# Optimization experiments

Measured on AMD Instinct MI355X. Metric: run time of the kernel, lower is better.

The kernel has to match this reference:

```python
import jax, jax.numpy as jnp
import numpy as np

N = 100000  # nodes
E = 1600000  # edges
F_IN = 512
H = 128
C = 40
L = 8
ALPHA = 0.1
THETA = 0.5


def setup_inputs() -> dict:
    key = jax.random.key(0)
    ks = jax.random.split(key, 8)
    x = jax.random.normal(ks[0], (N, F_IN), dtype=jnp.float32)
    edge_index = jax.random.randint(ks[1], (2, E), 0, N, dtype=jnp.int32)
    edge_weight = jax.random.uniform(ks[2], (E,), dtype=jnp.float32)
    W0 = jax.random.normal(ks[3], (F_IN, H), dtype=jnp.float32) * 0.05
    b0 = jnp.zeros((H,), dtype=jnp.float32)
    convW = jax.random.normal(ks[4], (L, H, H), dtype=jnp.float32) * 0.05
    W1 = jax.random.normal(ks[5], (H, C), dtype=jnp.float32) * 0.05
    b1 = jnp.zeros((C,), dtype=jnp.float32)
    return {"x": x, "edge_index": edge_index, "edge_weight": edge_weight,
            "W0": W0, "b0": b0, "convW": convW, "W1": W1, "b1": b1}


def reference(x, edge_index, edge_weight, W0, b0, convW, W1, b1):
    # eval mode, dropout=0.0 -> dropout is identity
    src, dst = edge_index[0], edge_index[1]
    h = jnp.maximum(x @ W0 + b0, 0.0)  # [N, H]
    x0 = h  # initial residual
    # GCN2Conv beta per layer: log(theta/layer + 1), layer = 1..L
    betas = jnp.log(THETA / jnp.arange(1, L + 1, dtype=jnp.float32) + 1.0)

    def layer(h, inputs):
        W, beta = inputs  # W: [H, H]
        # sparse adjacency propagation: sum_j A_ij * h_j
        msgs = h[src] * edge_weight[:, None]  # [E, H]
        agg = jax.ops.segment_sum(msgs, dst, num_segments=N)  # [N, H]
        # initial residual mixing + identity mapping (shared_weights=True)
        out = (1.0 - ALPHA) * agg + ALPHA * x0
        out = (1.0 - beta) * out + beta * (out @ W)
        return jnp.maximum(out, 0.0), None

    h, _ = jax.lax.scan(layer, h, (convW, betas))
    logits = h @ W1 + b1  # [N, C]
    return jax.nn.log_softmax(logits, axis=-1)
```

## Files before the change

### kernel.cpp

```cpp
#include <hip/hip_runtime.h>
#include <hip/hip_bf16.h>
#include <cmath>

#define NN 100000
#define NE 1600000
#define FIN 512
#define HD 128
#define NC 40
#define NL 8

typedef __attribute__((ext_vector_type(8))) short bh8;
typedef __attribute__((ext_vector_type(4))) float f4;
typedef __attribute__((ext_vector_type(4))) unsigned int u4;

__device__ __forceinline__ float bflo(unsigned p){ return __uint_as_float(p << 16); }
__device__ __forceinline__ float bfhi(unsigned p){ return __uint_as_float(p & 0xffff0000u); }
__device__ __forceinline__ unsigned short f2bf(float f){
  unsigned u = __float_as_uint(f);
  u += 0x7fffu + ((u >> 16) & 1u);
  return (unsigned short)(u >> 16);
}
__device__ __forceinline__ unsigned pack2(float a, float b){
  return (unsigned)f2bf(a) | ((unsigned)f2bf(b) << 16);
}

__global__ void k_deg(const int* __restrict__ dst, int* __restrict__ deg, int e){
  for (int i = blockIdx.x * blockDim.x + threadIdx.x; i < e; i += gridDim.x * blockDim.x)
    atomicAdd(&deg[dst[i]], 1);
}

__global__ void k_scan(const int* __restrict__ deg, int* __restrict__ offs,
                       int* __restrict__ cur, int n){
  __shared__ int wsum[16];
  __shared__ int carry;
  int t = threadIdx.x, lane = t & 63, wid = t >> 6;
  if (t == 0) carry = 0;
  __syncthreads();
  for (int base = 0; base < n; base += 1024){
    int idx = base + t;
    int v = (idx < n) ? deg[idx] : 0;
    int orig = v;
    #pragma unroll
    for (int off = 1; off < 64; off <<= 1){
      int u = __shfl_up(v, off);
      if (lane >= off) v += u;
    }
    if (lane == 63) wsum[wid] = v;
    __syncthreads();
    if (wid == 0){
      int s = (lane < 16) ? wsum[lane] : 0;
      #pragma unroll
      for (int off = 1; off < 16; off <<= 1){
        int u = __shfl_up(s, off);
        if (lane >= off) s += u;
      }
      if (lane < 16) wsum[lane] = s;
    }
    __syncthreads();
    int wexcl = (wid == 0) ? 0 : wsum[wid - 1];
    int excl = carry + wexcl + (v - orig);
    if (idx < n){ offs[idx] = excl; cur[idx] = excl; }
    int ctot = wsum[15];
    __syncthreads();
    if (t == 0) carry += ctot;
    __syncthreads();
  }
  if (t == 0) offs[n] = carry;
}

__global__ void k_scatter(const int* __restrict__ src, const int* __restrict__ dst,
                          const float* __restrict__ w, int* __restrict__ cur,
                          int* __restrict__ csrc, float* __restrict__ cw, int e){
  for (int i = blockIdx.x * blockDim.x + threadIdx.x; i < e; i += gridDim.x * blockDim.x){
    int d = dst[i];
    int p = atomicAdd(&cur[d], 1);
    csrc[p] = src[i];
    cw[p] = w[i];
  }
}

__global__ void k_twt(const float* __restrict__ in, unsigned short* __restrict__ out,
                      int K, int C, int Cpad){
  int total = Cpad * K;
  for (int i = blockIdx.x * blockDim.x + threadIdx.x; i < total; i += gridDim.x * blockDim.x){
    int c = i / K, k = i % K;
    float v = (c < C) ? in[(size_t)k * C + c] : 0.f;
    out[i] = f2bf(v);
  }
}

__global__ __launch_bounds__(256) void k_gemm0(const float* __restrict__ X,
                                               const unsigned short* __restrict__ Wt,
                                               const float* __restrict__ b0,
                                               unsigned* __restrict__ Ha,
                                               unsigned* __restrict__ Hb, int n){
  __shared__ __attribute__((aligned(16))) char lds[33792];
  char* ldsA = lds;
  char* ldsW = lds + 8192;
  float* ldsO = (float*)lds;
  int t = threadIdx.x;
  int w = t >> 6, lane = t & 63;
  int rowBase = blockIdx.x * 64;
  f4 acc[8];
  #pragma unroll
  for (int i = 0; i < 8; i++) acc[i] = (f4)0.f;

  for (int kk = 0; kk < 8; kk++){
    #pragma unroll
    for (int iter = 0; iter < 2; iter++){
      int r = t / 8 + iter * 32;
      int kc = (t % 8) * 8;
      int grow = rowBase + r;
      float4 f0 = {0,0,0,0}, f1 = {0,0,0,0};
      if (grow < n){
        const float4* p = (const float4*)(X + (size_t)grow * FIN + kk * 64 + kc);
        f0 = p[0]; f1 = p[1];
      }
      u4 pv = { pack2(f0.x, f0.y), pack2(f0.z, f0.w), pack2(f1.x, f1.y), pack2(f1.z, f1.w) };
      *(u4*)(ldsA + r * 128 + ((kc * 2) ^ ((r & 7) << 4))) = pv;
    }
    #pragma unroll
    for (int iter = 0; iter < 4; iter++){
      int c = t / 8 + iter * 32;
      int kc = (t % 8) * 8;
      bh8 v = *(const bh8*)(Wt + (size_t)c * FIN + kk * 64 + kc);
      *(bh8*)(ldsW + c * 128 + ((kc * 2) ^ ((c & 7) << 4))) = v;
    }
    __syncthreads();
    int rowf = (w << 4) + (lane & 15);
    #pragma unroll
    for (int ks = 0; ks < 2; ks++){
      bh8 fa = *(const bh8*)(ldsA + rowf * 128 + ((ks * 64 + (lane >> 4) * 16) ^ ((rowf & 7) << 4)));
      #pragma unroll
      for (int ct = 0; ct < 8; ct++){
        int colf = (ct << 4) + (lane & 15);
        bh8 fb = *(const bh8*)(ldsW + colf * 128 + ((ks * 64 + (lane >> 4) * 16) ^ ((colf & 7) << 4)));
        acc[ct] = __builtin_amdgcn_mfma_f32_16x16x32_bf16(fa, fb, acc[ct], 0, 0, 0);
      }
    }
    __syncthreads();
  }
  #pragma unroll
  for (int ct = 0; ct < 8; ct++){
    int colf = (ct << 4) + (lane & 15);
    float bb = b0[colf];
    #pragma unroll
    for (int i = 0; i < 4; i++){
      int r = (w << 4) + ((lane >> 4) << 2) + i;
      float v = acc[ct][i] + bb;
      ldsO[r * 132 + colf] = v > 0.f ? v : 0.f;
    }
  }
  __syncthreads();
  #pragma unroll
  for (int iter = 0; iter < 4; iter++){
    int r = iter * 16 + t / 16;
    int c8 = (t % 16) * 8;
    int grow = rowBase + r;
    if (grow < n){
      float* p = &ldsO[r * 132 + c8];
      u4 pv = { pack2(p[0], p[1]), pack2(p[2], p[3]), pack2(p[4], p[5]), pack2(p[6], p[7]) };
      *(u4*)(Ha + (size_t)grow * 64 + (t % 16) * 4) = pv;
      *(u4*)(Hb + (size_t)grow * 64 + (t % 16) * 4) = pv;
    }
  }
}

__global__ __launch_bounds__(256) void k_agg(const unsigned* __restrict__ H,
                                             const unsigned* __restrict__ X0,
                                             const int* __restrict__ offs,
                                             const int* __restrict__ csrc,
                                             const float* __restrict__ cw,
                                             unsigned* __restrict__ T, int n){
  int gw = (blockIdx.x * blockDim.x + threadIdx.x) >> 6;
  int lane = threadIdx.x & 63;
  int q = lane >> 4, l16 = lane & 15;
  int nw = (gridDim.x * blockDim.x) >> 6;
  for (int d = gw; d < n; d += nw){
    int e0 = offs[d], e1 = offs[d + 1];
    float a0=0.f,a1=0.f,a2=0.f,a3=0.f,a4=0.f,a5=0.f,a6=0.f,a7=0.f;
    for (int e = e0 + q; e < e1; e += 4){
      int s = csrc[e]; float wq = cw[e];
      u4 p = *(const u4*)(H + (size_t)s * 64 + l16 * 4);
      a0 += wq * bflo(p.x); a1 += wq * bfhi(p.x);
      a2 += wq * bflo(p.y); a3 += wq * bfhi(p.y);
      a4 += wq * bflo(p.z); a5 += wq * bfhi(p.z);
      a6 += wq * bflo(p.w); a7 += wq * bfhi(p.w);
    }
    a0 += __shfl_xor(a0,16); a0 += __shfl_xor(a0,32);
    a1 += __shfl_xor(a1,16); a1 += __shfl_xor(a1,32);
    a2 += __shfl_xor(a2,16); a2 += __shfl_xor(a2,32);
    a3 += __shfl_xor(a3,16); a3 += __shfl_xor(a3,32);
    a4 += __shfl_xor(a4,16); a4 += __shfl_xor(a4,32);
    a5 += __shfl_xor(a5,16); a5 += __shfl_xor(a5,32);
    a6 += __shfl_xor(a6,16); a6 += __shfl_xor(a6,32);
    a7 += __shfl_xor(a7,16); a7 += __shfl_xor(a7,32);
    if (q == 0){
      u4 xp = *(const u4*)(X0 + (size_t)d * 64 + l16 * 4);
      float v0 = 0.9f*a0 + 0.1f*bflo(xp.x), v1 = 0.9f*a1 + 0.1f*bfhi(xp.x);
      float v2 = 0.9f*a2 + 0.1f*bflo(xp.y), v3 = 0.9f*a3 + 0.1f*bfhi(xp.y);
      float v4 = 0.9f*a4 + 0.1f*bflo(xp.z), v5 = 0.9f*a5 + 0.1f*bfhi(xp.z);
      float v6 = 0.9f*a6 + 0.1f*bflo(xp.w), v7 = 0.9f*a7 + 0.1f*bfhi(xp.w);
      u4 ov = { pack2(v0,v1), pack2(v2,v3), pack2(v4,v5), pack2(v6,v7) };
      *(u4*)(T + (size_t)d * 64 + l16 * 4) = ov;
    }
  }
}

__global__ __launch_bounds__(256) void k_gemmL(const unsigned short* __restrict__ A,
                                               const unsigned short* __restrict__ Wt,
                                               float beta,
                                               unsigned* __restrict__ Hout, int n){
  __shared__ __attribute__((aligned(16))) char lds[49152];
  char* ldsA = lds;
  char* ldsW = lds + 16384;
  float* ldsO = (float*)lds;
  int t = threadIdx.x;
  int w = t >> 6, lane = t & 63;
  int rowBase = blockIdx.x * 64;

  #pragma unroll
  for (int iter = 0; iter < 4; iter++){
    int r = t / 16 + iter * 16;
    int kc = (t % 16) * 8;
    int grow = rowBase + r;
    bh8 v = (bh8)(short)0;
    if (grow < n) v = *(const bh8*)(A + (size_t)grow * HD + kc);
    *(bh8*)(ldsA + r * 256 + ((kc * 2) ^ ((r & 7) << 4))) = v;
  }
  #pragma unroll
  for (int iter = 0; iter < 8; iter++){
    int c = t / 16 + iter * 16;
    int kc = (t % 16) * 8;
    bh8 v = *(const bh8*)(Wt + (size_t)c * HD + kc);
    *(bh8*)(ldsW + c * 256 + ((kc * 2) ^ ((c & 7) << 4))) = v;
  }
  __syncthreads();

  f4 acc[8];
  #pragma unroll
  for (int i = 0; i < 8; i++) acc[i] = (f4)0.f;
  int rowf = (w << 4) + (lane & 15);
  #pragma unroll
  for (int ks = 0; ks < 4; ks++){
    bh8 fa = *(const bh8*)(ldsA + rowf * 256 + ((ks * 64 + (lane >> 4) * 16) ^ ((rowf & 7) << 4)));
    #pragma unroll
    for (int ct = 0; ct < 8; ct++){
      int colf = (ct << 4) + (lane & 15);
      bh8 fb = *(const bh8*)(ldsW + colf * 256 + ((ks * 64 + (lane >> 4) * 16) ^ ((colf & 7) << 4)));
      acc[ct] = __builtin_amdgcn_mfma_f32_16x16x32_bf16(fa, fb, acc[ct], 0, 0, 0);
    }
  }

  float vout[8][4];
  #pragma unroll
  for (int ct = 0; ct < 8; ct++){
    int colf = (ct << 4) + (lane & 15);
    #pragma unroll
    for (int i = 0; i < 4; i++){
      int r = (w << 4) + ((lane >> 4) << 2) + i;
      unsigned short tv = *(const unsigned short*)(ldsA + r * 256 + ((colf * 2) ^ ((r & 7) << 4)));
      float tf = __uint_as_float(((unsigned)tv) << 16);
      float v = (1.f - beta) * tf + beta * acc[ct][i];
      vout[ct][i] = v > 0.f ? v : 0.f;
    }
  }
  __syncthreads();
  #pragma unroll
  for (int ct = 0; ct < 8; ct++){
    int colf = (ct << 4) + (lane & 15);
    #pragma unroll
    for (int i = 0; i < 4; i++){
      int r = (w << 4) + ((lane >> 4) << 2) + i;
      ldsO[r * 132 + colf] = vout[ct][i];
    }
  }
  __syncthreads();
  #pragma unroll
  for (int iter = 0; iter < 4; iter++){
    int r = iter * 16 + t / 16;
    int c8 = (t % 16) * 8;
    int grow = rowBase + r;
    if (grow < n){
      float* p = &ldsO[r * 132 + c8];
      u4 pv = { pack2(p[0], p[1]), pack2(p[2], p[3]), pack2(p[4], p[5]), pack2(p[6], p[7]) };
      *(u4*)(Hout + (size_t)grow * 64 + (t % 16) * 4) = pv;
    }
  }
}

__global__ __launch_bounds__(256) void k_final(const unsigned* __restrict__ H,
                                               const unsigned short* __restrict__ W1t,
                                               const float* __restrict__ b1,
                                               float* __restrict__ out, int n){
  __shared__ __attribute__((aligned(16))) char lds[16384 + 12288];
  char* ldsA = lds;
  char* ldsW = lds + 16384;
  int t = threadIdx.x;
  int w = t >> 6, lane = t & 63;
  int l15 = lane & 15;
  int rowBase = blockIdx.x * 64;
  const unsigned short* Hs = (const unsigned short*)H;

  #pragma unroll
  for (int iter = 0; iter < 4; iter++){
    int r = t / 16 + iter * 16;
    int kc = (t % 16) * 8;
    int grow = rowBase + r;
    bh8 v = (bh8)(short)0;
    if (grow < n) v = *(const bh8*)(Hs + (size_t)grow * HD + kc);
    *(bh8*)(ldsA + r * 256 + ((kc * 2) ^ ((r & 7) << 4))) = v;
  }
  #pragma unroll
  for (int iter = 0; iter < 3; iter++){
    int c = t / 16 + iter * 16;
    int kc = (t % 16) * 8;
    bh8 v = *(const bh8*)(W1t + (size_t)c * HD + kc);
    *(bh8*)(ldsW + c * 256 + ((kc * 2) ^ ((c & 7) << 4))) = v;
  }
  __syncthreads();

  f4 acc[3];
  #pragma unroll
  for (int i = 0; i < 3; i++) acc[i] = (f4)0.f;
  int rowf = (w << 4) + l15;
  #pragma unroll
  for (int ks = 0; ks < 4; ks++){
    bh8 fa = *(const bh8*)(ldsA + rowf * 256 + ((ks * 64 + (lane >> 4) * 16) ^ ((rowf & 7) << 4)));
    #pragma unroll
    for (int ct = 0; ct < 3; ct++){
      int colf = (ct << 4) + l15;
      bh8 fb = *(const bh8*)(ldsW + colf * 256 + ((ks * 64 + (lane >> 4) * 16) ^ ((colf & 7) << 4)));
      acc[ct] = __builtin_amdgcn_mfma_f32_16x16x32_bf16(fa, fb, acc[ct], 0, 0, 0);
    }
  }

  float bias0 = b1[l15];
  float bias1 = b1[16 + l15];
  bool v2ok = (l15 < 8);
  float bias2 = v2ok ? b1[32 + l15] : 0.f;

  #pragma unroll
  for (int i = 0; i < 4; i++){
    int r = rowBase + (w << 4) + ((lane >> 4) << 2) + i;
    float v0 = acc[0][i] + bias0;
    float v1 = acc[1][i] + bias1;
    float v2 = v2ok ? (acc[2][i] + bias2) : -1e30f;
    float m = fmaxf(fmaxf(v0, v1), v2);
    #pragma unroll
    for (int off = 1; off < 16; off <<= 1) m = fmaxf(m, __shfl_xor(m, off));
    float e0 = __expf(v0 - m), e1 = __expf(v1 - m);
    float e2 = v2ok ? __expf(v2 - m) : 0.f;
    float s = e0 + e1 + e2;
    #pragma unroll
    for (int off = 1; off < 16; off <<= 1) s += __shfl_xor(s, off);
    float ls = m + __logf(s);
    if (r < n){
      out[(size_t)r * NC + l15] = v0 - ls;
      out[(size_t)r * NC + 16 + l15] = v1 - ls;
      if (v2ok) out[(size_t)r * NC + 32 + l15] = v2 - ls;
    }
  }
}

extern "C" void kernel_launch(void* const* d_in, const int* in_sizes, int n_in,
                              void* d_out, int out_size, void* d_ws, size_t ws_size,
                              hipStream_t stream){
  const float* x  = (const float*)d_in[0];
  const int*   ei = (const int*)d_in[1];
  const float* ew = (const float*)d_in[2];
  const float* W0 = (const float*)d_in[3];
  const float* b0 = (const float*)d_in[4];
  const float* cW = (const float*)d_in[5];
  const float* W1 = (const float*)d_in[6];
  const float* b1 = (const float*)d_in[7];
  float* out = (float*)d_out;
  const int* src = ei;
  const int* dst = ei + NE;

  char* ws = (char*)d_ws;
  size_t off = 0;
  auto alloc = [&](size_t bytes) -> char* {
    char* p = ws + off;
    off += (bytes + 255) & ~(size_t)255;
    return p;
  };
  unsigned* x0b = (unsigned*)alloc((size_t)NN * 64 * 4);
  unsigned* hb  = (unsigned*)alloc((size_t)NN * 64 * 4);
  unsigned* tb  = (unsigned*)alloc((size_t)NN * 64 * 4);
  unsigned short* W0t = (unsigned short*)alloc((size_t)FIN * HD * 2);
  unsigned short* cWt = (unsigned short*)alloc((size_t)NL * HD * HD * 2);
  unsigned short* W1t = (unsigned short*)alloc((size_t)48 * HD * 2);
  int*   deg  = (int*)alloc((size_t)NN * 4);
  int*   offs = (int*)alloc((size_t)(NN + 1) * 4);
  int*   cur  = (int*)alloc((size_t)NN * 4);
  int*   csrc = (int*)alloc((size_t)NE * 4);
  float* cwv  = (float*)alloc((size_t)NE * 4);

  (void)hipMemsetAsync(deg, 0, (size_t)NN * 4, stream);
  hipLaunchKernelGGL(k_deg, dim3(1024), dim3(256), 0, stream, dst, deg, NE);
  hipLaunchKernelGGL(k_scan, dim3(1), dim3(1024), 0, stream, deg, offs, cur, NN);
  hipLaunchKernelGGL(k_scatter, dim3(1024), dim3(256), 0, stream, src, dst, ew, cur, csrc, cwv, NE);
  hipLaunchKernelGGL(k_twt, dim3(256), dim3(256), 0, stream, W0, W0t, FIN, HD, HD);
  for (int l = 0; l < NL; l++)
    hipLaunchKernelGGL(k_twt, dim3(64), dim3(256), 0, stream,
                       cW + (size_t)l * HD * HD, cWt + (size_t)l * HD * HD, HD, HD, HD);
  hipLaunchKernelGGL(k_twt, dim3(24), dim3(256), 0, stream, W1, W1t, HD, NC, 48);

  int gblocks = (NN + 63) / 64;
  hipLaunchKernelGGL(k_gemm0, dim3(gblocks), dim3(256), 0, stream, x, W0t, b0, x0b, hb, NN);
  for (int l = 0; l < NL; l++){
    float beta = logf(0.5f / (float)(l + 1) + 1.0f);
    hipLaunchKernelGGL(k_agg, dim3(2048), dim3(256), 0, stream, hb, x0b, offs, csrc, cwv, tb, NN);
    hipLaunchKernelGGL(k_gemmL, dim3(gblocks), dim3(256), 0, stream,
                       (const unsigned short*)tb, cWt + (size_t)l * HD * HD, beta, hb, NN);
  }
  hipLaunchKernelGGL(k_final, dim3(gblocks), dim3(256), 0, stream, hb, W1t, b1, out, NN);
}
```

Baseline: 1.049 ms.

## Fuse sparse aggregation into per-layer GEMM kernel and pack edge src/weight

Merges the per-layer aggregation and dense GEMM into one kernel. Each block aggregates its 64 rows straight into LDS, then runs the MFMA GEMM with ping-pong H buffers, so the intermediate T tensor is never written to or read back from global memory. Edge source index and weight are packed into one 8-byte record, and the gather loop is unrolled by two to keep more loads in flight. The trade-off is a fixed 64-rows-per-block schedule instead of a grid-stride warp loop, which can cause load imbalance across blocks and lower occupancy from the larger LDS footprint.

```diff
diff --git a/kernel.cpp b/kernel.cpp
--- a/kernel.cpp
+++ b/kernel.cpp
@@ -12,6 +12,7 @@
 typedef __attribute__((ext_vector_type(8))) short bh8;
 typedef __attribute__((ext_vector_type(4))) float f4;
 typedef __attribute__((ext_vector_type(4))) unsigned int u4;
+typedef __attribute__((ext_vector_type(2))) unsigned int u2;
 
 __device__ __forceinline__ float bflo(unsigned p){ return __uint_as_float(p << 16); }
 __device__ __forceinline__ float bfhi(unsigned p){ return __uint_as_float(p & 0xffff0000u); }
@@ -70,12 +71,12 @@
 
 __global__ void k_scatter(const int* __restrict__ src, const int* __restrict__ dst,
                           const float* __restrict__ w, int* __restrict__ cur,
-                          int* __restrict__ csrc, float* __restrict__ cw, int e){
+                          u2* __restrict__ epk, int e){
   for (int i = blockIdx.x * blockDim.x + threadIdx.x; i < e; i += gridDim.x * blockDim.x){
     int d = dst[i];
     int p = atomicAdd(&cur[d], 1);
-    csrc[p] = src[i];
-    cw[p] = w[i];
+    u2 v = { (unsigned)src[i], __float_as_uint(w[i]) };
+    epk[p] = v;
   }
 }
 
@@ -166,26 +167,59 @@
   }
 }
 
-__global__ __launch_bounds__(256) void k_agg(const unsigned* __restrict__ H,
-                                             const unsigned* __restrict__ X0,
-                                             const int* __restrict__ offs,
-                                             const int* __restrict__ csrc,
-                                             const float* __restrict__ cw,
-                                             unsigned* __restrict__ T, int n){
-  int gw = (blockIdx.x * blockDim.x + threadIdx.x) >> 6;
-  int lane = threadIdx.x & 63;
+__global__ __launch_bounds__(256) void k_layer(const unsigned* __restrict__ Hin,
+                                               const unsigned* __restrict__ X0,
+                                               const int* __restrict__ offs,
+                                               const u2* __restrict__ epk,
+                                               const unsigned short* __restrict__ Wt,
+                                               float beta,
+                                               unsigned* __restrict__ Hout, int n){
+  __shared__ __attribute__((aligned(16))) char lds[49152];
+  char* ldsA = lds;
+  char* ldsW = lds + 16384;
+  float* ldsO = (float*)lds;
+  int t = threadIdx.x;
+  int w = t >> 6, lane = t & 63;
   int q = lane >> 4, l16 = lane & 15;
-  int nw = (gridDim.x * blockDim.x) >> 6;
-  for (int d = gw; d < n; d += nw){
+  int rowBase = blockIdx.x * 64;
+
+  #pragma unroll
+  for (int iter = 0; iter < 8; iter++){
+    int c = t / 16 + iter * 16;
+    int kc = (t % 16) * 8;
+    bh8 v = *(const bh8*)(Wt + (size_t)c * HD + kc);
+    *(bh8*)(ldsW + c * 256 + ((kc * 2) ^ ((c & 7) << 4))) = v;
+  }
+
+  for (int i = 0; i < 16; i++){
+    int lr = (w << 4) + i;
+    int d = rowBase + lr;
+    if (d >= n) continue;
     int e0 = offs[d], e1 = offs[d + 1];
     float a0=0.f,a1=0.f,a2=0.f,a3=0.f,a4=0.f,a5=0.f,a6=0.f,a7=0.f;
-    for (int e = e0 + q; e < e1; e += 4){
-      int s = csrc[e]; float wq = cw[e];
-      u4 p = *(const u4*)(H + (size_t)s * 64 + l16 * 4);
-      a0 += wq * bflo(p.x); a1 += wq * bfhi(p.x);
-      a2 += wq * bflo(p.y); a3 += wq * bfhi(p.y);
-      a4 += wq * bflo(p.z); a5 += wq * bfhi(p.z);
-      a6 += wq * bflo(p.w); a7 += wq * bfhi(p.w);
+    int e = e0 + q;
+    for (; e + 4 < e1; e += 8){
+      u2 p0 = epk[e], p1 = epk[e + 4];
+      float w0 = __uint_as_float(p0.y), w1 = __uint_as_float(p1.y);
+      u4 r0 = *(const u4*)(Hin + (size_t)p0.x * 64 + l16 * 4);
+      u4 r1 = *(const u4*)(Hin + (size_t)p1.x * 64 + l16 * 4);
+      a0 += w0 * bflo(r0.x) + w1 * bflo(r1.x);
+      a1 += w0 * bfhi(r0.x) + w1 * bfhi(r1.x);
+      a2 += w0 * bflo(r0.y) + w1 * bflo(r1.y);
+      a3 += w0 * bfhi(r0.y) + w1 * bfhi(r1.y);
+      a4 += w0 * bflo(r0.z) + w1 * bflo(r1.z);
+      a5 += w0 * bfhi(r0.z) + w1 * bfhi(r1.z);
+      a6 += w0 * bflo(r0.w) + w1 * bflo(r1.w);
+      a7 += w0 * bfhi(r0.w) + w1 * bfhi(r1.w);
+    }
+    if (e < e1){
+      u2 p0 = epk[e];
+      float w0 = __uint_as_float(p0.y);
+      u4 r0 = *(const u4*)(Hin + (size_t)p0.x * 64 + l16 * 4);
+      a0 += w0 * bflo(r0.x); a1 += w0 * bfhi(r0.x);
+      a2 += w0 * bflo(r0.y); a3 += w0 * bfhi(r0.y);
+      a4 += w0 * bflo(r0.z); a5 += w0 * bfhi(r0.z);
+      a6 += w0 * bflo(r0.w); a7 += w0 * bfhi(r0.w);
     }
     a0 += __shfl_xor(a0,16); a0 += __shfl_xor(a0,32);
     a1 += __shfl_xor(a1,16); a1 += __shfl_xor(a1,32);
@@ -202,38 +236,8 @@
       float v4 = 0.9f*a4 + 0.1f*bflo(xp.z), v5 = 0.9f*a5 + 0.1f*bfhi(xp.z);
       float v6 = 0.9f*a6 + 0.1f*bflo(xp.w), v7 = 0.9f*a7 + 0.1f*bfhi(xp.w);
       u4 ov = { pack2(v0,v1), pack2(v2,v3), pack2(v4,v5), pack2(v6,v7) };
-      *(u4*)(T + (size_t)d * 64 + l16 * 4) = ov;
-    }
-  }
-}
-
-__global__ __launch_bounds__(256) void k_gemmL(const unsigned short* __restrict__ A,
-                                               const unsigned short* __restrict__ Wt,
-                                               float beta,
-                                               unsigned* __restrict__ Hout, int n){
-  __shared__ __attribute__((aligned(16))) char lds[49152];
-  char* ldsA = lds;
-  char* ldsW = lds + 16384;
-  float* ldsO = (float*)lds;
-  int t = threadIdx.x;
-  int w = t >> 6, lane = t & 63;
-  int rowBase = blockIdx.x * 64;
-
-  #pragma unroll
-  for (int iter = 0; iter < 4; iter++){
-    int r = t / 16 + iter * 16;
-    int kc = (t % 16) * 8;
-    int grow = rowBase + r;
-    bh8 v = (bh8)(short)0;
-    if (grow < n) v = *(const bh8*)(A + (size_t)grow * HD + kc);
-    *(bh8*)(ldsA + r * 256 + ((kc * 2) ^ ((r & 7) << 4))) = v;
-  }
-  #pragma unroll
-  for (int iter = 0; iter < 8; iter++){
-    int c = t / 16 + iter * 16;
-    int kc = (t % 16) * 8;
-    bh8 v = *(const bh8*)(Wt + (size_t)c * HD + kc);
-    *(bh8*)(ldsW + c * 256 + ((kc * 2) ^ ((c & 7) << 4))) = v;
+      *(u4*)(ldsA + lr * 256 + ((l16 * 16) ^ ((lr & 7) << 4))) = ov;
+    }
   }
   __syncthreads();
 
@@ -386,21 +390,20 @@
     return p;
   };
   unsigned* x0b = (unsigned*)alloc((size_t)NN * 64 * 4);
-  unsigned* hb  = (unsigned*)alloc((size_t)NN * 64 * 4);
-  unsigned* tb  = (unsigned*)alloc((size_t)NN * 64 * 4);
+  unsigned* hbA = (unsigned*)alloc((size_t)NN * 64 * 4);
+  unsigned* hbB = (unsigned*)alloc((size_t)NN * 64 * 4);
   unsigned short* W0t = (unsigned short*)alloc((size_t)FIN * HD * 2);
   unsigned short* cWt = (unsigned short*)alloc((size_t)NL * HD * HD * 2);
   unsigned short* W1t = (unsigned short*)alloc((size_t)48 * HD * 2);
   int*   deg  = (int*)alloc((size_t)NN * 4);
   int*   offs = (int*)alloc((size_t)(NN + 1) * 4);
   int*   cur  = (int*)alloc((size_t)NN * 4);
-  int*   csrc = (int*)alloc((size_t)NE * 4);
-  float* cwv  = (float*)alloc((size_t)NE * 4);
+  u2*    epk  = (u2*)alloc((size_t)NE * 8);
 
   (void)hipMemsetAsync(deg, 0, (size_t)NN * 4, stream);
   hipLaunchKernelGGL(k_deg, dim3(1024), dim3(256), 0, stream, dst, deg, NE);
   hipLaunchKernelGGL(k_scan, dim3(1), dim3(1024), 0, stream, deg, offs, cur, NN);
-  hipLaunchKernelGGL(k_scatter, dim3(1024), dim3(256), 0, stream, src, dst, ew, cur, csrc, cwv, NE);
+  hipLaunchKernelGGL(k_scatter, dim3(1024), dim3(256), 0, stream, src, dst, ew, cur, epk, NE);
   hipLaunchKernelGGL(k_twt, dim3(256), dim3(256), 0, stream, W0, W0t, FIN, HD, HD);
   for (int l = 0; l < NL; l++)
     hipLaunchKernelGGL(k_twt, dim3(64), dim3(256), 0, stream,
@@ -408,12 +411,13 @@
   hipLaunchKernelGGL(k_twt, dim3(24), dim3(256), 0, stream, W1, W1t, HD, NC, 48);
 
   int gblocks = (NN + 63) / 64;
-  hipLaunchKernelGGL(k_gemm0, dim3(gblocks), dim3(256), 0, stream, x, W0t, b0, x0b, hb, NN);
+  hipLaunchKernelGGL(k_gemm0, dim3(gblocks), dim3(256), 0, stream, x, W0t, b0, x0b, hbA, NN);
   for (int l = 0; l < NL; l++){
     float beta = logf(0.5f / (float)(l + 1) + 1.0f);
-    hipLaunchKernelGGL(k_agg, dim3(2048), dim3(256), 0, stream, hb, x0b, offs, csrc, cwv, tb, NN);
-    hipLaunchKernelGGL(k_gemmL, dim3(gblocks), dim3(256), 0, stream,
-                       (const unsigned short*)tb, cWt + (size_t)l * HD * HD, beta, hb, NN);
-  }
-  hipLaunchKernelGGL(k_final, dim3(gblocks), dim3(256), 0, stream, hb, W1t, b1, out, NN);
-}
+    const unsigned* hin = (l & 1) ? hbB : hbA;
+    unsigned* hout = (l & 1) ? hbA : hbB;
+    hipLaunchKernelGGL(k_layer, dim3(gblocks), dim3(256), 0, stream,
+                       hin, x0b, offs, epk, cWt + (size_t)l * HD * HD, beta, hout, NN);
+  }
+  hipLaunchKernelGGL(k_final, dim3(gblocks), dim3(256), 0, stream, hbA, W1t, b1, out, NN);
+}
```

Result: slower. 1.490 ms (+42.0%).
